# Performance work log

Measured on AMD Instinct MI355X. Metric: run time of the kernel, lower is better.

## Reference

```python
import jax, jax.numpy as jnp
import numpy as np


def squash(v, axis=-1):
    # scale = |v|^2 / (1+|v|^2) / |v|, applied elementwise along `axis`
    s2 = jnp.sum(jnp.square(v), axis=axis, keepdims=True)
    scale = s2 / (1.0 + s2) / jnp.sqrt(s2)
    return scale * v


def setup_inputs() -> dict:
    key = jax.random.key(0)
    k1, k2 = jax.random.split(key)
    B, I, D_in = 128, 1152, 8   # batch, input_num_capsule, input_dim_vector
    N, D_out = 32, 16           # num_capsule, dim_vector
    inputs = jax.random.normal(k1, (B, I, D_in), dtype=jnp.float32)
    # glorot_uniform-like scale for W: [in_caps, num_caps, in_dim, out_dim]
    limit = np.sqrt(6.0 / (D_in + D_out)).astype(np.float32)
    W = jax.random.uniform(k2, (I, N, D_in, D_out), dtype=jnp.float32,
                           minval=-limit, maxval=limit)
    bias = jnp.zeros((1, I, N), dtype=jnp.float32)  # routing logits (zeros init)
    return {"inputs": inputs, "W": W, "bias": bias}


def reference(inputs, W, bias):
    num_routing = 3
    # inputs_hat[b,i,n,e] = sum_d inputs[b,i,d] * W[i,n,d,e]
    # (the original's tf.scan over batch + batch_dot is just this einsum)
    u_hat = jnp.einsum('bid,inde->bine', inputs, W)  # [B,I,N,E]

    b = jnp.broadcast_to(bias, u_hat.shape[:3])  # [B,I,N] (bias broadcasts over batch)
    outputs = None
    for it in range(num_routing):
        c = jax.nn.softmax(b, axis=2)                       # softmax over num_capsule
        s = jnp.einsum('bin,bine->bne', c, u_hat)           # weighted sum over in_caps
        outputs = squash(s, axis=-1)                        # [B,N,E]
        if it != num_routing - 1:
            # agreement update: b += <u_hat, v>
            b = b + jnp.einsum('bine,bne->bin', u_hat, outputs)
    return outputs  # [B, num_capsule, dim_vector]
```

## Files before the change

### kernel.cpp

```cpp
#include <hip/hip_runtime.h>
#include <hip/hip_fp16.h>

namespace {

constexpr int kB = 128, kI = 1152, kD = 8, kN = 32, kE = 16;
constexpr int kTI = 4;
constexpr int kNC = kI / kTI;
constexpr int kCG = 4;
constexpr int kCPG = kNC / kCG;

constexpr size_t kPartBytes  = (size_t)kNC * kB * kN * kE * 2;
constexpr size_t kPart2Bytes = (size_t)kCG * kB * kN * kE * 4;
constexpr size_t kVsumBytes  = (size_t)kB * kN * kE * 4;

typedef _Float16 h2v __attribute__((ext_vector_type(2)));

__device__ __forceinline__ float fdot2(__half2 a, __half2 b, float c) {
#if defined(__has_builtin) && __has_builtin(__builtin_amdgcn_fdot2)
  return __builtin_amdgcn_fdot2(__builtin_bit_cast(h2v, a),
                                __builtin_bit_cast(h2v, b), c, false);
#else
  float2 af = __half22float2(a), bf = __half22float2(b);
  return fmaf(af.y, bf.y, fmaf(af.x, bf.x, c));
#endif
}

union I4H { int4 v; __half2 h[4]; };

template<int PASS>
__global__ __launch_bounds__(256, 2)
void caps_pass(const float* __restrict__ x, const float* __restrict__ W,
               const float* __restrict__ bias, const __half* __restrict__ vsh,
               __half* __restrict__ part)
{
  __shared__ __half2 xlds[32][kTI * kD];

  const int chunk = (int)blockIdx.x;
  const int i0 = chunk * kTI;
  const int b0 = (int)blockIdx.y * 32;
  const int t = (int)threadIdx.x;
  const int lane = t & 63;
  const int wv = t >> 6;
  const int eh = lane >> 5;
  const int n  = lane & 31;

  {
    const int r = t >> 3, c = (t & 7) * 4;
    const float4 f4 = *reinterpret_cast<const float4*>(
        x + (size_t)(b0 + r) * (kI * kD) + (size_t)i0 * kD + c);
    xlds[r][c + 0] = __half2half2(__float2half_rn(f4.x));
    xlds[r][c + 1] = __half2half2(__float2half_rn(f4.y));
    xlds[r][c + 2] = __half2half2(__float2half_rn(f4.z));
    xlds[r][c + 3] = __half2half2(__float2half_rn(f4.w));
  }

  __half2 wr[kTI][kD][4];
  {
    const float* wb = W + ((size_t)i0 * kN + n) * (kD * kE) + eh * 8;
#pragma unroll
    for (int i = 0; i < kTI; ++i)
#pragma unroll
      for (int d = 0; d < kD; ++d) {
        const float4* p = reinterpret_cast<const float4*>(
            wb + (size_t)i * (kN * kD * kE) + d * kE);
        float4 a = p[0], b4 = p[1];
        wr[i][d][0] = __floats2half2_rn(a.x, a.y);
        wr[i][d][1] = __floats2half2_rn(a.z, a.w);
        wr[i][d][2] = __floats2half2_rn(b4.x, b4.y);
        wr[i][d][3] = __floats2half2_rn(b4.z, b4.w);
      }
  }

  float bf[kTI];
#pragma unroll
  for (int i = 0; i < kTI; ++i) bf[i] = bias[(size_t)(i0 + i) * kN + n];

  __half2 c0[kTI];
  if (PASS == 0) {
#pragma unroll
    for (int i = 0; i < kTI; ++i) {
      float lg = bf[i];
      float m = lg;
#pragma unroll
      for (int o = 1; o <= 16; o <<= 1) m = fmaxf(m, __shfl_xor(m, o, 64));
      float ev = __expf(lg - m);
      float sm = ev;
#pragma unroll
      for (int o = 1; o <= 16; o <<= 1) sm += __shfl_xor(sm, o, 64);
      c0[i] = __half2half2(__float2half_rn(ev / sm));
    }
  }

  __syncthreads();

#pragma unroll 2
  for (int bb = 0; bb < 8; ++bb) {
    const int bl = wv * 8 + bb;
    const int b = b0 + bl;
    I4H vq;
    if (PASS > 0)
      vq.v = *reinterpret_cast<const int4*>(vsh + ((size_t)b * kN + n) * kE + eh * 8);

    __half2 s[4];
#pragma unroll
    for (int k = 0; k < 4; ++k) s[k] = __half2half2(__float2half(0.f));

#pragma unroll
    for (int i = 0; i < kTI; ++i) {
      I4H xa, xb;
      xa.v = *reinterpret_cast<const int4*>(&xlds[bl][i * kD]);
      xb.v = *reinterpret_cast<const int4*>(&xlds[bl][i * kD + 4]);
      __half2 uh[4];
#pragma unroll
      for (int k = 0; k < 4; ++k) uh[k] = __hmul2(xa.h[0], wr[i][0][k]);
#pragma unroll
      for (int d = 1; d < 4; ++d)
#pragma unroll
        for (int k = 0; k < 4; ++k) uh[k] = __hfma2(xa.h[d], wr[i][d][k], uh[k]);
#pragma unroll
      for (int d = 0; d < 4; ++d)
#pragma unroll
        for (int k = 0; k < 4; ++k) uh[k] = __hfma2(xb.h[d], wr[i][4 + d][k], uh[k]);

      __half2 c2;
      if (PASS == 0) {
        c2 = c0[i];
      } else {
        float lg = bf[i];
#pragma unroll
        for (int k = 0; k < 4; ++k) lg = fdot2(uh[k], vq.h[k], lg);
        lg += __shfl_xor(lg, 32, 64);
        float m = lg;
#pragma unroll
        for (int o = 1; o <= 16; o <<= 1) m = fmaxf(m, __shfl_xor(m, o, 64));
        float ev = __expf(lg - m);
        float sm = ev;
#pragma unroll
        for (int o = 1; o <= 16; o <<= 1) sm += __shfl_xor(sm, o, 64);
        c2 = __half2half2(__float2half_rn(ev / sm));
      }
#pragma unroll
      for (int k = 0; k < 4; ++k) s[k] = __hfma2(c2, uh[k], s[k]);
    }
    I4H o;
#pragma unroll
    for (int k = 0; k < 4; ++k) o.h[k] = s[k];
    *reinterpret_cast<int4*>(
        part + (((size_t)chunk * kB + b) * kN + n) * kE + eh * 8) = o.v;
  }
}

__global__ __launch_bounds__(256)
void caps_reduce1(const __half* __restrict__ part, float* __restrict__ partial2)
{
  const int cg = (int)blockIdx.y;
  const int t = (int)threadIdx.x;
  const int b = (int)blockIdx.x * 4 + (t >> 6);
  const int l = t & 63;
  const __half* p0 = part + ((size_t)(cg * kCPG) * kB + b) * (kN * kE) + l * 8;
  constexpr size_t chStride = (size_t)kB * kN * kE;
  float acc[8] = {0.f, 0.f, 0.f, 0.f, 0.f, 0.f, 0.f, 0.f};
#pragma unroll 4
  for (int ch = 0; ch < kCPG; ++ch) {
    I4H q; q.v = *reinterpret_cast<const int4*>(p0 + (size_t)ch * chStride);
#pragma unroll
    for (int k = 0; k < 4; ++k) {
      float2 f = __half22float2(q.h[k]);
      acc[2 * k] += f.x; acc[2 * k + 1] += f.y;
    }
  }
  float* dst = partial2 + ((size_t)cg * kB + b) * (kN * kE) + l * 8;
  *reinterpret_cast<float4*>(dst)     = make_float4(acc[0], acc[1], acc[2], acc[3]);
  *reinterpret_cast<float4*>(dst + 4) = make_float4(acc[4], acc[5], acc[6], acc[7]);
}

template<int MODE>
__global__ __launch_bounds__(256)
void caps_final(const float* __restrict__ partial2, float* __restrict__ vsum,
                __half* __restrict__ vsh, float* __restrict__ out)
{
  const int b = (int)blockIdx.x;
  const int t = (int)threadIdx.x;
  const int nl = t >> 3, ep = t & 7;
  const size_t o = ((size_t)b * kN + nl) * kE + ep * 2;
  float ax = 0.f, ay = 0.f;
#pragma unroll
  for (int cg = 0; cg < kCG; ++cg) {
    float2 f = *reinterpret_cast<const float2*>(
        partial2 + (size_t)cg * kB * kN * kE + o);
    ax += f.x; ay += f.y;
  }
  float s2 = ax * ax + ay * ay;
  s2 += __shfl_xor(s2, 1, 64);
  s2 += __shfl_xor(s2, 2, 64);
  s2 += __shfl_xor(s2, 4, 64);
  const float sc = (s2 / (1.f + s2)) * rsqrtf(fmaxf(s2, 1e-30f));
  float vx = ax * sc, vy = ay * sc;
  if (MODE == 2) {
    *reinterpret_cast<float2*>(out + o) = make_float2(vx, vy);
  } else {
    if (MODE == 1) {
      float2 old = *reinterpret_cast<const float2*>(vsum + o);
      vx += old.x; vy += old.y;
    }
    *reinterpret_cast<float2*>(vsum + o) = make_float2(vx, vy);
    *reinterpret_cast<__half2*>(vsh + o) = __floats2half2_rn(vx, vy);
  }
}

}

extern "C" void kernel_launch(void* const* d_in, const int* in_sizes, int n_in,
                              void* d_out, int out_size, void* d_ws, size_t ws_size,
                              hipStream_t stream) {
  (void)in_sizes; (void)n_in; (void)out_size; (void)ws_size;
  const float* x    = reinterpret_cast<const float*>(d_in[0]);
  const float* W    = reinterpret_cast<const float*>(d_in[1]);
  const float* bias = reinterpret_cast<const float*>(d_in[2]);
  float* out = reinterpret_cast<float*>(d_out);

  char* ws = reinterpret_cast<char*>(d_ws);
  __half* part     = reinterpret_cast<__half*>(ws);
  float*  partial2 = reinterpret_cast<float*>(ws + kPartBytes);
  float*  vsum     = reinterpret_cast<float*>(ws + kPartBytes + kPart2Bytes);
  __half* vsh      = reinterpret_cast<__half*>(ws + kPartBytes + kPart2Bytes + kVsumBytes);

  dim3 pg(kNC, kB / 32), pb(256);
  dim3 rg(kB / 4, kCG), rb(256);

  caps_pass<0><<<pg, pb, 0, stream>>>(x, W, bias, vsh, part);
  caps_reduce1<<<rg, rb, 0, stream>>>(part, partial2);
  caps_final<0><<<kB, 256, 0, stream>>>(partial2, vsum, vsh, out);
  caps_pass<1><<<pg, pb, 0, stream>>>(x, W, bias, vsh, part);
  caps_reduce1<<<rg, rb, 0, stream>>>(part, partial2);
  caps_final<1><<<kB, 256, 0, stream>>>(partial2, vsum, vsh, out);
  caps_pass<2><<<pg, pb, 0, stream>>>(x, W, bias, vsh, part);
  caps_reduce1<<<rg, rb, 0, stream>>>(part, partial2);
  caps_final<2><<<kB, 256, 0, stream>>>(partial2, vsum, vsh, out);
}
```

Baseline: 255.4 us.

## Stage W through swizzled LDS and accumulate 8 input capsules per block

Each pass block now covers 8 input capsules and 16 batch rows, looping over 4 sub-chunks of 2 capsules. Each sub-chunk's W is loaded with coalesced reads, converted to half and stored in an XOR-swizzled LDS tile, then copied into registers. The partial sums stay in registers across sub-chunks, which cuts the number of fp16 partial outputs and the reduce traffic by half. The change also moves bias into LDS, replaces the softmax division with a hardware reciprocal, raises occupancy to 3, and in later passes recomputes u_hat instead of keeping it in registers. The costs are more barriers per block, recomputing u_hat twice, and the same W being reloaded by more blocks along the batch axis.

```diff
diff --git a/kernel.cpp b/kernel.cpp
--- a/kernel.cpp
+++ b/kernel.cpp
@@ -4,12 +4,14 @@
 namespace {
 
 constexpr int kB = 128, kI = 1152, kD = 8, kN = 32, kE = 16;
-constexpr int kTI = 4;
-constexpr int kNC = kI / kTI;
-constexpr int kCG = 4;
-constexpr int kCPG = kNC / kCG;
-
-constexpr size_t kPartBytes  = (size_t)kNC * kB * kN * kE * 2;
+constexpr int kTI = 2;
+constexpr int kCH = 4;
+constexpr int kIB = kTI * kCH;
+constexpr int kNG = kI / kIB;
+constexpr int kCG = 6;
+constexpr int kGPG = kNG / kCG;
+
+constexpr size_t kPartBytes  = (size_t)kNG * kB * kN * kE * 2;
 constexpr size_t kPart2Bytes = (size_t)kCG * kB * kN * kE * 4;
 constexpr size_t kVsumBytes  = (size_t)kB * kN * kE * 4;
 
@@ -25,128 +27,184 @@
 #endif
 }
 
+__device__ __forceinline__ float frcp(float v) {
+#if defined(__has_builtin) && __has_builtin(__builtin_amdgcn_rcpf)
+  return __builtin_amdgcn_rcpf(v);
+#else
+  return 1.0f / v;
+#endif
+}
+
 union I4H { int4 v; __half2 h[4]; };
 
+__device__ __forceinline__ void keep(int4& v) {
+  asm volatile("" : "+v"(v.x), "+v"(v.y), "+v"(v.z), "+v"(v.w));
+}
+
+__device__ __forceinline__ void uh_comp(const __half2* __restrict__ xp,
+                                        const I4H* __restrict__ wrow,
+                                        __half2 uh[4]) {
+  I4H xa, xb;
+  xa.v = reinterpret_cast<const int4*>(xp)[0];
+  xb.v = reinterpret_cast<const int4*>(xp)[1];
+#pragma unroll
+  for (int k = 0; k < 4; ++k) uh[k] = __hmul2(xa.h[0], wrow[0].h[k]);
+#pragma unroll
+  for (int d = 1; d < 4; ++d)
+#pragma unroll
+    for (int k = 0; k < 4; ++k) uh[k] = __hfma2(xa.h[d], wrow[d].h[k], uh[k]);
+#pragma unroll
+  for (int d = 0; d < 4; ++d)
+#pragma unroll
+    for (int k = 0; k < 4; ++k) uh[k] = __hfma2(xb.h[d], wrow[4 + d].h[k], uh[k]);
+}
+
 template<int PASS>
-__global__ __launch_bounds__(256, 2)
+__global__ __launch_bounds__(256, 3)
 void caps_pass(const float* __restrict__ x, const float* __restrict__ W,
                const float* __restrict__ bias, const __half* __restrict__ vsh,
                __half* __restrict__ part)
 {
-  __shared__ __half2 xlds[32][kTI * kD];
-
-  const int chunk = (int)blockIdx.x;
-  const int i0 = chunk * kTI;
-  const int b0 = (int)blockIdx.y * 32;
-  const int t = (int)threadIdx.x;
-  const int lane = t & 63;
+  __shared__ int4    wlds[kTI * kD * 64];
+  __shared__ __half2 xlds[16][kIB * kD];
+  __shared__ float   blds[kIB * kN];
+
+  const int g  = (int)blockIdx.x;
+  const int g0 = g * kIB;
+  const int b0 = (int)blockIdx.y * 16;
+  const int t  = (int)threadIdx.x;
+  const int L  = t & 63;
   const int wv = t >> 6;
-  const int eh = lane >> 5;
-  const int n  = lane & 31;
+  const int eh = L >> 5;
+  const int n  = L & 31;
 
   {
-    const int r = t >> 3, c = (t & 7) * 4;
+    const int br = t >> 4, q = t & 15;
     const float4 f4 = *reinterpret_cast<const float4*>(
-        x + (size_t)(b0 + r) * (kI * kD) + (size_t)i0 * kD + c);
-    xlds[r][c + 0] = __half2half2(__float2half_rn(f4.x));
-    xlds[r][c + 1] = __half2half2(__float2half_rn(f4.y));
-    xlds[r][c + 2] = __half2half2(__float2half_rn(f4.z));
-    xlds[r][c + 3] = __half2half2(__float2half_rn(f4.w));
-  }
-
-  __half2 wr[kTI][kD][4];
-  {
-    const float* wb = W + ((size_t)i0 * kN + n) * (kD * kE) + eh * 8;
+        x + (size_t)(b0 + br) * (kI * kD) + (size_t)g0 * kD + q * 4);
+    xlds[br][q * 4 + 0] = __half2half2(__float2half_rn(f4.x));
+    xlds[br][q * 4 + 1] = __half2half2(__float2half_rn(f4.y));
+    xlds[br][q * 4 + 2] = __half2half2(__float2half_rn(f4.z));
+    xlds[br][q * 4 + 3] = __half2half2(__float2half_rn(f4.w));
+    blds[t] = bias[(size_t)g0 * kN + t];
+  }
+
+  __half2 sAcc[4][4];
+#pragma unroll
+  for (int bb = 0; bb < 4; ++bb)
+#pragma unroll
+    for (int k = 0; k < 4; ++k) sAcc[bb][k] = __half2half2(__float2half(0.f));
+
+#pragma unroll 1
+  for (int s = 0; s < kCH; ++s) {
+    __syncthreads();
+    {
+      const float* wsrc = W + (size_t)(g0 + s * kTI) * (kN * kD * kE);
+#pragma unroll
+      for (int j = 0; j < 8; ++j) {
+        const int f = (j * 256 + t) * 4;
+        const float4 w4 = *reinterpret_cast<const float4*>(wsrc + f);
+        const int il = f >> 12, rem = f & 4095;
+        const int nn = rem >> 7, dd = (rem >> 4) & 7, e = rem & 15;
+        const int r = il * 8 + dd;
+        const int col = (((e >> 3) << 5) + nn) ^ (r & 7);
+        __half2* wh = reinterpret_cast<__half2*>(&wlds[r * 64 + col]);
+        const int pp = (e & 7) >> 1;
+        wh[pp]     = __floats2half2_rn(w4.x, w4.y);
+        wh[pp + 1] = __floats2half2_rn(w4.z, w4.w);
+      }
+    }
+    __syncthreads();
+    I4H wreg[kTI][kD];
 #pragma unroll
     for (int i = 0; i < kTI; ++i)
 #pragma unroll
       for (int d = 0; d < kD; ++d) {
-        const float4* p = reinterpret_cast<const float4*>(
-            wb + (size_t)i * (kN * kD * kE) + d * kE);
-        float4 a = p[0], b4 = p[1];
-        wr[i][d][0] = __floats2half2_rn(a.x, a.y);
-        wr[i][d][1] = __floats2half2_rn(a.z, a.w);
-        wr[i][d][2] = __floats2half2_rn(b4.x, b4.y);
-        wr[i][d][3] = __floats2half2_rn(b4.z, b4.w);
-      }
-  }
-
-  float bf[kTI];
-#pragma unroll
-  for (int i = 0; i < kTI; ++i) bf[i] = bias[(size_t)(i0 + i) * kN + n];
-
-  __half2 c0[kTI];
-  if (PASS == 0) {
-#pragma unroll
-    for (int i = 0; i < kTI; ++i) {
-      float lg = bf[i];
-      float m = lg;
-#pragma unroll
-      for (int o = 1; o <= 16; o <<= 1) m = fmaxf(m, __shfl_xor(m, o, 64));
-      float ev = __expf(lg - m);
-      float sm = ev;
-#pragma unroll
-      for (int o = 1; o <= 16; o <<= 1) sm += __shfl_xor(sm, o, 64);
-      c0[i] = __half2half2(__float2half_rn(ev / sm));
-    }
-  }
-
-  __syncthreads();
-
-#pragma unroll 2
-  for (int bb = 0; bb < 8; ++bb) {
-    const int bl = wv * 8 + bb;
-    const int b = b0 + bl;
-    I4H vq;
-    if (PASS > 0)
-      vq.v = *reinterpret_cast<const int4*>(vsh + ((size_t)b * kN + n) * kE + eh * 8);
-
-    __half2 s[4];
-#pragma unroll
-    for (int k = 0; k < 4; ++k) s[k] = __half2half2(__float2half(0.f));
-
-#pragma unroll
-    for (int i = 0; i < kTI; ++i) {
-      I4H xa, xb;
-      xa.v = *reinterpret_cast<const int4*>(&xlds[bl][i * kD]);
-      xb.v = *reinterpret_cast<const int4*>(&xlds[bl][i * kD + 4]);
-      __half2 uh[4];
-#pragma unroll
-      for (int k = 0; k < 4; ++k) uh[k] = __hmul2(xa.h[0], wr[i][0][k]);
-#pragma unroll
-      for (int d = 1; d < 4; ++d)
-#pragma unroll
-        for (int k = 0; k < 4; ++k) uh[k] = __hfma2(xa.h[d], wr[i][d][k], uh[k]);
-#pragma unroll
-      for (int d = 0; d < 4; ++d)
-#pragma unroll
-        for (int k = 0; k < 4; ++k) uh[k] = __hfma2(xb.h[d], wr[i][4 + d][k], uh[k]);
-
-      __half2 c2;
-      if (PASS == 0) {
-        c2 = c0[i];
-      } else {
-        float lg = bf[i];
-#pragma unroll
-        for (int k = 0; k < 4; ++k) lg = fdot2(uh[k], vq.h[k], lg);
-        lg += __shfl_xor(lg, 32, 64);
+        const int r = i * 8 + d;
+        wreg[i][d].v = wlds[r * 64 + (L ^ (r & 7))];
+        keep(wreg[i][d].v);
+      }
+
+    if (PASS == 0) {
+      __half2 c0[kTI];
+#pragma unroll
+      for (int i = 0; i < kTI; ++i) {
+        const float lg = blds[(s * kTI + i) * kN + n];
         float m = lg;
 #pragma unroll
         for (int o = 1; o <= 16; o <<= 1) m = fmaxf(m, __shfl_xor(m, o, 64));
-        float ev = __expf(lg - m);
+        const float ev = __expf(lg - m);
         float sm = ev;
 #pragma unroll
         for (int o = 1; o <= 16; o <<= 1) sm += __shfl_xor(sm, o, 64);
-        c2 = __half2half2(__float2half_rn(ev / sm));
-      }
-#pragma unroll
-      for (int k = 0; k < 4; ++k) s[k] = __hfma2(c2, uh[k], s[k]);
-    }
+        c0[i] = __half2half2(__float2half_rn(ev * frcp(sm)));
+      }
+#pragma unroll
+      for (int bb = 0; bb < 4; ++bb) {
+        const int bl = wv * 4 + bb;
+#pragma unroll
+        for (int i = 0; i < kTI; ++i) {
+          __half2 uh[4];
+          uh_comp(&xlds[bl][(s * kTI + i) * kD], wreg[i], uh);
+#pragma unroll
+          for (int k = 0; k < 4; ++k) sAcc[bb][k] = __hfma2(c0[i], uh[k], sAcc[bb][k]);
+        }
+      }
+    } else {
+      float lgv[4][kTI];
+#pragma unroll
+      for (int bb = 0; bb < 4; ++bb) {
+        const int bl = wv * 4 + bb;
+        I4H vq;
+        vq.v = *reinterpret_cast<const int4*>(
+            vsh + ((size_t)(b0 + bl) * kN + n) * kE + eh * 8);
+#pragma unroll
+        for (int i = 0; i < kTI; ++i) {
+          __half2 uh[4];
+          uh_comp(&xlds[bl][(s * kTI + i) * kD], wreg[i], uh);
+          float lg = blds[(s * kTI + i) * kN + n];
+#pragma unroll
+          for (int k = 0; k < 4; ++k) lg = fdot2(uh[k], vq.h[k], lg);
+          lg += __shfl_xor(lg, 32, 64);
+          lgv[bb][i] = lg;
+        }
+      }
+      __half2 cc[4][kTI];
+#pragma unroll
+      for (int bb = 0; bb < 4; ++bb)
+#pragma unroll
+        for (int i = 0; i < kTI; ++i) {
+          float m = lgv[bb][i];
+#pragma unroll
+          for (int o = 1; o <= 16; o <<= 1) m = fmaxf(m, __shfl_xor(m, o, 64));
+          const float ev = __expf(lgv[bb][i] - m);
+          float sm = ev;
+#pragma unroll
+          for (int o = 1; o <= 16; o <<= 1) sm += __shfl_xor(sm, o, 64);
+          cc[bb][i] = __half2half2(__float2half_rn(ev * frcp(sm)));
+        }
+#pragma unroll
+      for (int bb = 0; bb < 4; ++bb) {
+        const int bl = wv * 4 + bb;
+#pragma unroll
+        for (int i = 0; i < kTI; ++i) {
+          __half2 uh[4];
+          uh_comp(&xlds[bl][(s * kTI + i) * kD], wreg[i], uh);
+#pragma unroll
+          for (int k = 0; k < 4; ++k) sAcc[bb][k] = __hfma2(cc[bb][i], uh[k], sAcc[bb][k]);
+        }
+      }
+    }
+  }
+
+#pragma unroll
+  for (int bb = 0; bb < 4; ++bb) {
+    const int b = b0 + wv * 4 + bb;
     I4H o;
 #pragma unroll
-    for (int k = 0; k < 4; ++k) o.h[k] = s[k];
+    for (int k = 0; k < 4; ++k) o.h[k] = sAcc[bb][k];
     *reinterpret_cast<int4*>(
-        part + (((size_t)chunk * kB + b) * kN + n) * kE + eh * 8) = o.v;
+        part + (((size_t)g * kB + b) * kN + n) * kE + eh * 8) = o.v;
   }
 }
 
@@ -157,12 +215,12 @@
   const int t = (int)threadIdx.x;
   const int b = (int)blockIdx.x * 4 + (t >> 6);
   const int l = t & 63;
-  const __half* p0 = part + ((size_t)(cg * kCPG) * kB + b) * (kN * kE) + l * 8;
-  constexpr size_t chStride = (size_t)kB * kN * kE;
+  const __half* p0 = part + ((size_t)(cg * kGPG) * kB + b) * (kN * kE) + l * 8;
+  constexpr size_t gStride = (size_t)kB * kN * kE;
   float acc[8] = {0.f, 0.f, 0.f, 0.f, 0.f, 0.f, 0.f, 0.f};
 #pragma unroll 4
-  for (int ch = 0; ch < kCPG; ++ch) {
-    I4H q; q.v = *reinterpret_cast<const int4*>(p0 + (size_t)ch * chStride);
+  for (int ch = 0; ch < kGPG; ++ch) {
+    I4H q; q.v = *reinterpret_cast<const int4*>(p0 + (size_t)ch * gStride);
 #pragma unroll
     for (int k = 0; k < 4; ++k) {
       float2 f = __half22float2(q.h[k]);
@@ -225,7 +283,7 @@
   float*  vsum     = reinterpret_cast<float*>(ws + kPartBytes + kPart2Bytes);
   __half* vsh      = reinterpret_cast<__half*>(ws + kPartBytes + kPart2Bytes + kVsumBytes);
 
-  dim3 pg(kNC, kB / 32), pb(256);
+  dim3 pg(kNG, kB / 16), pb(256);
   dim3 rg(kB / 4, kCG), rb(256);
 
   caps_pass<0><<<pg, pb, 0, stream>>>(x, W, bias, vsh, part);
```

Measured after the change: 392.7 us. +53.7%, slower.

## Stage W through swizzled LDS with coalesced loads; batch softmax across input capsules

Applied to the files above, without the earlier changes.

W is now loaded by all threads with fully coalesced float4 reads into a bank-swizzled shared-memory tile, then each thread pulls its fp16 weights from LDS, replacing strided per-thread global loads. The routing passes restructure the inner loop to compute all u_hat and logits first and then run the four softmax shuffle reductions together, which exposes more independent work. Division is replaced with a hardware reciprocal approximation, and the batch loop is no longer unrolled. This adds 32KB LDS per block, which may limit occupancy.

```diff
diff --git a/kernel.cpp b/kernel.cpp
--- a/kernel.cpp
+++ b/kernel.cpp
@@ -25,7 +25,37 @@
 #endif
 }
 
+__device__ __forceinline__ float frcp(float v) {
+#if defined(__has_builtin) && __has_builtin(__builtin_amdgcn_rcpf)
+  return __builtin_amdgcn_rcpf(v);
+#else
+  return 1.0f / v;
+#endif
+}
+
 union I4H { int4 v; __half2 h[4]; };
+
+__device__ __forceinline__ void keep(int4& v) {
+  asm volatile("" : "+v"(v.x), "+v"(v.y), "+v"(v.z), "+v"(v.w));
+}
+
+__device__ __forceinline__ void uh_comp(const __half2* __restrict__ xp,
+                                        const I4H* __restrict__ wrow,
+                                        __half2 uh[4]) {
+  I4H xa, xb;
+  xa.v = reinterpret_cast<const int4*>(xp)[0];
+  xb.v = reinterpret_cast<const int4*>(xp)[1];
+#pragma unroll
+  for (int k = 0; k < 4; ++k) uh[k] = __hmul2(xa.h[0], wrow[0].h[k]);
+#pragma unroll
+  for (int d = 1; d < 4; ++d)
+#pragma unroll
+    for (int k = 0; k < 4; ++k) uh[k] = __hfma2(xa.h[d], wrow[d].h[k], uh[k]);
+#pragma unroll
+  for (int d = 0; d < 4; ++d)
+#pragma unroll
+    for (int k = 0; k < 4; ++k) uh[k] = __hfma2(xb.h[d], wrow[4 + d].h[k], uh[k]);
+}
 
 template<int PASS>
 __global__ __launch_bounds__(256, 2)
@@ -33,16 +63,17 @@
                const float* __restrict__ bias, const __half* __restrict__ vsh,
                __half* __restrict__ part)
 {
+  __shared__ int4    wlds[kTI * kD * 64];
   __shared__ __half2 xlds[32][kTI * kD];
 
   const int chunk = (int)blockIdx.x;
   const int i0 = chunk * kTI;
   const int b0 = (int)blockIdx.y * 32;
-  const int t = (int)threadIdx.x;
-  const int lane = t & 63;
+  const int t  = (int)threadIdx.x;
+  const int L  = t & 63;
   const int wv = t >> 6;
-  const int eh = lane >> 5;
-  const int n  = lane & 31;
+  const int eh = L >> 5;
+  const int n  = L & 31;
 
   {
     const int r = t >> 3, c = (t & 7) * 4;
@@ -53,23 +84,33 @@
     xlds[r][c + 2] = __half2half2(__float2half_rn(f4.z));
     xlds[r][c + 3] = __half2half2(__float2half_rn(f4.w));
   }
-
-  __half2 wr[kTI][kD][4];
   {
-    const float* wb = W + ((size_t)i0 * kN + n) * (kD * kE) + eh * 8;
-#pragma unroll
-    for (int i = 0; i < kTI; ++i)
-#pragma unroll
-      for (int d = 0; d < kD; ++d) {
-        const float4* p = reinterpret_cast<const float4*>(
-            wb + (size_t)i * (kN * kD * kE) + d * kE);
-        float4 a = p[0], b4 = p[1];
-        wr[i][d][0] = __floats2half2_rn(a.x, a.y);
-        wr[i][d][1] = __floats2half2_rn(a.z, a.w);
-        wr[i][d][2] = __floats2half2_rn(b4.x, b4.y);
-        wr[i][d][3] = __floats2half2_rn(b4.z, b4.w);
-      }
-  }
+    const float* wsrc = W + (size_t)i0 * (kN * kD * kE);
+#pragma unroll
+    for (int j = 0; j < 16; ++j) {
+      const int f = (j * 256 + t) * 4;
+      const float4 w4 = *reinterpret_cast<const float4*>(wsrc + f);
+      const int il = f >> 12, rem = f & 4095;
+      const int nn = rem >> 7, dd = (rem >> 4) & 7, e = rem & 15;
+      const int r = il * 8 + dd;
+      const int col = (((e >> 3) << 5) + nn) ^ (r & 7);
+      __half2* wh = reinterpret_cast<__half2*>(&wlds[r * 64 + col]);
+      const int pp = (e & 7) >> 1;
+      wh[pp]     = __floats2half2_rn(w4.x, w4.y);
+      wh[pp + 1] = __floats2half2_rn(w4.z, w4.w);
+    }
+  }
+  __syncthreads();
+
+  I4H wreg[kTI][kD];
+#pragma unroll
+  for (int i = 0; i < kTI; ++i)
+#pragma unroll
+    for (int d = 0; d < kD; ++d) {
+      const int r = i * 8 + d;
+      wreg[i][d].v = wlds[r * 64 + (L ^ (r & 7))];
+      keep(wreg[i][d].v);
+    }
 
   float bf[kTI];
 #pragma unroll
@@ -79,69 +120,67 @@
   if (PASS == 0) {
 #pragma unroll
     for (int i = 0; i < kTI; ++i) {
-      float lg = bf[i];
-      float m = lg;
+      float m = bf[i];
 #pragma unroll
       for (int o = 1; o <= 16; o <<= 1) m = fmaxf(m, __shfl_xor(m, o, 64));
-      float ev = __expf(lg - m);
+      const float ev = __expf(bf[i] - m);
       float sm = ev;
 #pragma unroll
       for (int o = 1; o <= 16; o <<= 1) sm += __shfl_xor(sm, o, 64);
-      c0[i] = __half2half2(__float2half_rn(ev / sm));
-    }
-  }
-
-  __syncthreads();
-
-#pragma unroll 2
+      c0[i] = __half2half2(__float2half_rn(ev * frcp(sm)));
+    }
+  }
+
+#pragma unroll 1
   for (int bb = 0; bb < 8; ++bb) {
     const int bl = wv * 8 + bb;
     const int b = b0 + bl;
-    I4H vq;
-    if (PASS > 0)
-      vq.v = *reinterpret_cast<const int4*>(vsh + ((size_t)b * kN + n) * kE + eh * 8);
 
     __half2 s[4];
 #pragma unroll
     for (int k = 0; k < 4; ++k) s[k] = __half2half2(__float2half(0.f));
 
-#pragma unroll
-    for (int i = 0; i < kTI; ++i) {
-      I4H xa, xb;
-      xa.v = *reinterpret_cast<const int4*>(&xlds[bl][i * kD]);
-      xb.v = *reinterpret_cast<const int4*>(&xlds[bl][i * kD + 4]);
-      __half2 uh[4];
-#pragma unroll
-      for (int k = 0; k < 4; ++k) uh[k] = __hmul2(xa.h[0], wr[i][0][k]);
-#pragma unroll
-      for (int d = 1; d < 4; ++d)
-#pragma unroll
-        for (int k = 0; k < 4; ++k) uh[k] = __hfma2(xa.h[d], wr[i][d][k], uh[k]);
-#pragma unroll
-      for (int d = 0; d < 4; ++d)
-#pragma unroll
-        for (int k = 0; k < 4; ++k) uh[k] = __hfma2(xb.h[d], wr[i][4 + d][k], uh[k]);
-
-      __half2 c2;
-      if (PASS == 0) {
-        c2 = c0[i];
-      } else {
+    if (PASS == 0) {
+#pragma unroll
+      for (int i = 0; i < kTI; ++i) {
+        __half2 uh[4];
+        uh_comp(&xlds[bl][i * kD], wreg[i], uh);
+#pragma unroll
+        for (int k = 0; k < 4; ++k) s[k] = __hfma2(c0[i], uh[k], s[k]);
+      }
+    } else {
+      I4H vq;
+      vq.v = *reinterpret_cast<const int4*>(
+          vsh + ((size_t)b * kN + n) * kE + eh * 8);
+      __half2 uhs[kTI][4];
+      float lgv[kTI];
+#pragma unroll
+      for (int i = 0; i < kTI; ++i) {
+        uh_comp(&xlds[bl][i * kD], wreg[i], uhs[i]);
         float lg = bf[i];
 #pragma unroll
-        for (int k = 0; k < 4; ++k) lg = fdot2(uh[k], vq.h[k], lg);
+        for (int k = 0; k < 4; ++k) lg = fdot2(uhs[i][k], vq.h[k], lg);
         lg += __shfl_xor(lg, 32, 64);
-        float m = lg;
+        lgv[i] = lg;
+      }
+      __half2 cc[kTI];
+#pragma unroll
+      for (int i = 0; i < kTI; ++i) {
+        float m = lgv[i];
 #pragma unroll
         for (int o = 1; o <= 16; o <<= 1) m = fmaxf(m, __shfl_xor(m, o, 64));
-        float ev = __expf(lg - m);
+        const float ev = __expf(lgv[i] - m);
         float sm = ev;
 #pragma unroll
         for (int o = 1; o <= 16; o <<= 1) sm += __shfl_xor(sm, o, 64);
-        c2 = __half2half2(__float2half_rn(ev / sm));
+        cc[i] = __half2half2(__float2half_rn(ev * frcp(sm)));
       }
 #pragma unroll
-      for (int k = 0; k < 4; ++k) s[k] = __hfma2(c2, uh[k], s[k]);
-    }
+      for (int i = 0; i < kTI; ++i)
+#pragma unroll
+        for (int k = 0; k < 4; ++k) s[k] = __hfma2(cc[i], uhs[i][k], s[k]);
+    }
+
     I4H o;
 #pragma unroll
     for (int k = 0; k < 4; ++k) o.h[k] = s[k];
```

After: 224.0 us. -12.3%, faster.
